# Optimization experiments

Measured on AMD Instinct MI355X. Metric: run time of the kernel, lower is better.

## Reference

```python
import jax, jax.numpy as jnp
import numpy as np

VOCAB = 32000
H = 256
B = 4
S = 512


def setup_inputs() -> dict:
    key = jax.random.key(0)
    ks = jax.random.split(key, 12)
    s = 1.0 / np.sqrt(H)
    inp = {
        "x": jax.random.randint(ks[0], (B, S), 0, VOCAB),
        "embed": jax.random.normal(ks[1], (VOCAB, H), jnp.float32) * 0.02,
        "Wi": jax.random.normal(ks[2], (H, H), jnp.float32) * s,   # i2h weight (in,out)
        "bi": jax.random.normal(ks[3], (H,), jnp.float32) * s,
        "Wh": jax.random.normal(ks[4], (H, H), jnp.float32) * s,   # h2h weight
        "bh": jax.random.normal(ks[5], (H,), jnp.float32) * s,
        "Wa": jax.random.normal(ks[6], (2 * H, H), jnp.float32) * s,  # attn_W (in=2H,out=H)
        "ba": jax.random.normal(ks[7], (H,), jnp.float32) * s,
        "va": jax.random.normal(ks[8], (H,), jnp.float32) * s,     # attn_v (no bias)
        "Wo": jax.random.normal(ks[9], (H, VOCAB), jnp.float32) * s,  # fc_out
        "bo": jax.random.normal(ks[10], (VOCAB,), jnp.float32) * s,
    }
    return inp


def _forward(x, embed, Wi, bi, Wh, bh, Wa, ba, va, Wo, bo):
    emb = embed[x]                               # [B,S,H]
    h0 = jnp.zeros((x.shape[0], H), emb.dtype)

    def step(h, e_t):
        h_new = jnp.tanh(e_t @ Wi + bi + h @ Wh + bh)
        return h_new, h_new

    _, hs = jax.lax.scan(step, h0, jnp.swapaxes(emb, 0, 1))  # [S,B,H]
    enc = jnp.swapaxes(hs, 0, 1)                 # [B,S,H] encoder states

    # Additive attention: energy(t,s) = tanh(W[ h_t ; h_s ] + b), score = v . energy
    Wq, Wk = Wa[:H], Wa[H:]
    q = enc @ Wq                                 # [B,S,H] (query = h_t half)
    k = enc @ Wk                                 # [B,S,H] (history half)
    energy = jnp.tanh(q[:, :, None, :] + k[:, None, :, :] + ba)  # [B,T,S,H]
    scores = jnp.einsum("btsh,h->bts", energy, va)

    seq = x.shape[1]
    causal = jnp.arange(seq)[None, :] < jnp.arange(seq)[:, None]  # [T,S]: s < t strictly
    weights = jax.nn.softmax(jnp.where(causal[None], scores, -1e9), axis=-1)
    ctx = jnp.einsum("bts,bsh->bth", weights, enc)               # [B,S,H]
    # t == 0: context = h_0 itself (no history)
    ctx = jnp.where((jnp.arange(seq) == 0)[None, :, None], enc[:, 0:1, :], ctx)

    out = (ctx + enc) @ Wo + bo                  # [B,S,V]
    return out, enc[:, -1, :]


def reference(x, embed, Wi, bi, Wh, bh, Wa, ba, va, Wo, bo):
    return _forward(x, embed, Wi, bi, Wh, bh, Wa, ba, va, Wo, bo)
```

## Files before the change

kernel.cpp:

```cpp
#include <hip/hip_runtime.h>
#include <hip/hip_bf16.h>
#include <hip/hip_fp16.h>

#define VOCAB 32000
#define H 256
#define B 4
#define S 512

typedef _Float16 f16x8 __attribute__((ext_vector_type(8)));
typedef short s16x8 __attribute__((ext_vector_type(8)));
typedef float f32x4 __attribute__((ext_vector_type(4)));

__device__ __forceinline__ float tanh_fast(float x) {
    float e = exp2f(x * 2.885390081777927f);
    return 1.0f - 2.0f * __builtin_amdgcn_rcpf(e + 1.0f);
}

__device__ __forceinline__ size_t fragIdx(int row, int h) {
    return ((size_t)((((row >> 4) * 8 + (h >> 5)) * 64) + ((h >> 3) & 3) * 16 + (row & 15)) << 3)
           + (h & 7);
}

__global__ __launch_bounds__(256) void k_wot(const float* __restrict__ Wo,
                                             ushort* __restrict__ WoTF) {
    __shared__ float tile[256][65];
    int n0 = blockIdx.x * 64;
    int tx = threadIdx.x & 63, ty = threadIdx.x >> 6;
#pragma unroll
    for (int i = 0; i < 64; ++i) {
        int k = i * 4 + ty;
        tile[k][tx] = Wo[(size_t)k * VOCAB + n0 + tx];
    }
    __syncthreads();
#pragma unroll
    for (int r = 0; r < 8; ++r) {
        int lin = threadIdx.x + 256 * r;
        int ll = lin & 15, lg = (lin >> 4) & 3, kk = (lin >> 6) & 7, nt = lin >> 9;
        int n = nt * 16 + ll;
        s16x8 v;
#pragma unroll
        for (int e = 0; e < 8; ++e) {
            __hip_bfloat16 b = __float2bfloat16(tile[kk * 32 + lg * 8 + e][n]);
            v[e] = *(short*)&b;
        }
        size_t unit = (size_t)(((n0 >> 4) + nt) * 8 + kk) * 64 + lg * 16 + ll;
        *(s16x8*)&WoTF[unit * 8] = v;
    }
}

__global__ void k_eprep(const int* __restrict__ x, const float* __restrict__ embed,
                        const float* __restrict__ Wi, const float* __restrict__ bi,
                        const float* __restrict__ bh, float* __restrict__ Ew) {
    int t = blockIdx.x, j = threadIdx.x;
    __shared__ float es[B][H];
    __shared__ int xs[B];
    if (j < B) xs[j] = x[j * S + t];
    __syncthreads();
    for (int b = 0; b < B; ++b) es[b][j] = embed[(size_t)xs[b] * H + j];
    float bias = bi[j] + bh[j];
    float a0 = bias, a1 = bias, a2 = bias, a3 = bias;
    __syncthreads();
    for (int i = 0; i < H; ++i) {
        float w = Wi[i * H + j];
        a0 += es[0][i] * w; a1 += es[1][i] * w;
        a2 += es[2][i] * w; a3 += es[3][i] * w;
    }
    f32x4 v; v[0] = a0; v[1] = a1; v[2] = a2; v[3] = a3;
    *(f32x4*)&Ew[(t * H + j) * 4] = v;
}

__global__ __launch_bounds__(256, 1) void k_rnn(const float* __restrict__ Ew,
                                                const float* __restrict__ Wh,
                                                _Float16* __restrict__ enc16,
                                                float* __restrict__ out_tail) {
    const int tid = threadIdx.x;
    const int w = tid >> 6;
    const int l = tid & 63;
    const int lg = l >> 4;
    const int ll = l & 15;

    __shared__ _Float16 hbuf[2][4][258];
    for (int idx = tid; idx < 2 * 4 * 258; idx += 256) (&hbuf[0][0][0])[idx] = (_Float16)0.f;

    f16x8 Bf[4][8];
#pragma unroll
    for (int nt = 0; nt < 4; ++nt) {
        int col = w * 64 + nt * 16 + ll;
#pragma unroll
        for (int kk = 0; kk < 8; ++kk) {
            int kb = kk * 32 + lg * 8;
            f16x8 v;
#pragma unroll
            for (int e = 0; e < 8; ++e) v[e] = (_Float16)Wh[(kb + e) * H + col];
            Bf[nt][kk] = v;
        }
    }
    __syncthreads();

    f32x4 eacc[2][4];
#pragma unroll
    for (int d = 0; d < 2; ++d)
#pragma unroll
        for (int nt = 0; nt < 4; ++nt) {
            int j = w * 64 + nt * 16 + ll;
            eacc[d][nt] = *(const f32x4*)&Ew[(d * H + j) * 4];
        }

    const int jcol = w * 64 + lg * 16 + ll;

    for (int t0 = 0; t0 < S; t0 += 2) {
#pragma unroll
        for (int u = 0; u < 2; ++u) {
            const int t = t0 + u;
            const int cur = u, nxt = u ^ 1;

            f16x8 Af[8];
#pragma unroll
            for (int kk = 0; kk < 8; ++kk)
                Af[kk] = *(const f16x8*)&hbuf[cur][l & 3][kk * 32 + lg * 8];

            f32x4 acc[4];
#pragma unroll
            for (int nt = 0; nt < 4; ++nt) acc[nt] = eacc[u][nt];

            {
                int tp = (t + 2 < S) ? t + 2 : S - 1;
#pragma unroll
                for (int nt = 0; nt < 4; ++nt) {
                    int j = w * 64 + nt * 16 + ll;
                    eacc[u][nt] = *(const f32x4*)&Ew[(tp * H + j) * 4];
                }
            }

#pragma unroll
            for (int kk = 0; kk < 8; ++kk)
#pragma unroll
                for (int nt = 0; nt < 4; ++nt)
                    acc[nt] = __builtin_amdgcn_mfma_f32_16x16x32_f16(Af[kk], Bf[nt][kk], acc[nt], 0, 0, 0);

            float v[4];
#pragma unroll
            for (int nt = 0; nt < 4; ++nt)
#pragma unroll
                for (int r = 0; r < 4; ++r) {
                    float tv = __shfl(acc[nt][r], ll);
                    if (lg == nt) v[r] = tv;
                }

            float hv[4];
#pragma unroll
            for (int r = 0; r < 4; ++r) hv[r] = tanh_fast(v[r]);

#pragma unroll
            for (int r = 0; r < 4; ++r) {
                _Float16 h16 = (_Float16)hv[r];
                hbuf[nxt][r][jcol] = h16;
                enc16[(r * S + t) * H + jcol] = h16;
            }
            if (t == S - 1) {
#pragma unroll
                for (int r = 0; r < 4; ++r) out_tail[r * H + jcol] = hv[r];
            }

            asm volatile("s_waitcnt lgkmcnt(0)" ::: "memory");
            __builtin_amdgcn_s_barrier();
            asm volatile("" ::: "memory");
        }
    }
}

__global__ void k_qk(const _Float16* __restrict__ enc16, const float* __restrict__ Wa,
                     const float* __restrict__ ba, float* __restrict__ q,
                     float* __restrict__ kT) {
    int r0 = blockIdx.x * 8;
    int j = threadIdx.x;
    __shared__ float es[8][H];
#pragma unroll
    for (int r = 0; r < 8; ++r) es[r][j] = (float)enc16[(r0 + r) * H + j];
    __syncthreads();
    float aq[8] = {0, 0, 0, 0, 0, 0, 0, 0};
    float ak[8] = {0, 0, 0, 0, 0, 0, 0, 0};
    for (int i = 0; i < H; ++i) {
        float wq = Wa[i * H + j];
        float wk = Wa[(H + i) * H + j];
#pragma unroll
        for (int r = 0; r < 8; ++r) { aq[r] += es[r][i] * wq; ak[r] += es[r][i] * wk; }
    }
    float bav = ba[j];
#pragma unroll
    for (int r = 0; r < 8; ++r) {
        int row = r0 + r;
        int b = row >> 9, t = row & (S - 1);
        q[row * H + j] = aq[r];
        kT[((b * H + j) << 9) + t] = ak[r] + bav;
    }
}

__global__ void k_attn(const float* __restrict__ q, const float* __restrict__ kT,
                       const _Float16* __restrict__ enc16, const float* __restrict__ va,
                       ushort* __restrict__ AbfF) {
    int bt = blockIdx.x;
    int b = bt >> 9, t = bt & (S - 1);
    int tid = threadIdx.x;
    if (t == 0) {
        float e = (float)enc16[(b * S) * H + tid];
        __hip_bfloat16 bf = __float2bfloat16(2.0f * e);
        AbfF[fragIdx(bt, tid)] = *(ushort*)&bf;
        return;
    }
    __shared__ float qs[H], vas[H], part[4][S], wgt[S], red[8];
    qs[tid] = q[bt * H + tid];
    vas[tid] = va[tid];
    __syncthreads();

    int sl = tid & 63, g = tid >> 6;
    int nchunk = (t + 63) >> 6;
    const float* kTb = kT + ((size_t)(b * H) << 9);
    for (int c = 0; c < nchunk; ++c) {
        int s = c * 64 + sl;
        float p = 0.f;
        if (s < t) {
            int hb = g * 64;
            for (int i = 0; i < 64; ++i) {
                int h = hb + i;
                p += vas[h] * tanh_fast(qs[h] + kTb[(h << 9) + s]);
            }
        }
        part[g][s] = p;
    }
    __syncthreads();

    float m = -1e30f;
    for (int s = tid; s < t; s += 256) {
        float sc = part[0][s] + part[1][s] + part[2][s] + part[3][s];
        wgt[s] = sc;
        m = fmaxf(m, sc);
    }
#pragma unroll
    for (int off = 32; off; off >>= 1) m = fmaxf(m, __shfl_xor(m, off));
    if ((tid & 63) == 0) red[g] = m;
    __syncthreads();
    m = fmaxf(fmaxf(red[0], red[1]), fmaxf(red[2], red[3]));
    float ssum = 0.f;
    for (int s = tid; s < t; s += 256) {
        float e = exp2f((wgt[s] - m) * 1.4426950408889634f);
        wgt[s] = e;
        ssum += e;
    }
#pragma unroll
    for (int off = 32; off; off >>= 1) ssum += __shfl_xor(ssum, off);
    if ((tid & 63) == 0) red[4 + g] = ssum;
    __syncthreads();
    float inv = 1.0f / (red[4] + red[5] + red[6] + red[7]);

    float ctx = 0.f;
    const _Float16* eb = enc16 + (size_t)(b * S) * H + tid;
    for (int s = 0; s < t; ++s) ctx += wgt[s] * (float)eb[s * H];
    float et = (float)enc16[(b * S + t) * H + tid];
    __hip_bfloat16 bf = __float2bfloat16(ctx * inv + et);
    AbfF[fragIdx(bt, tid)] = *(ushort*)&bf;
}

__global__ __launch_bounds__(256) void k_out(const ushort* __restrict__ AbfF,
                                             const ushort* __restrict__ WoTF,
                                             const float* __restrict__ bo,
                                             float* __restrict__ out) {
    int tid = threadIdx.x;
    int wv = tid >> 6, l = tid & 63;
    int mw = wv >> 1, nw = wv & 1;
    int lg = l >> 4, ll = l & 15;
    int m0 = blockIdx.y * 128 + mw * 64;
    int n0 = blockIdx.x * 128 + nw * 64;

    f32x4 acc[4][4];
#pragma unroll
    for (int mt = 0; mt < 4; ++mt)
#pragma unroll
        for (int nt = 0; nt < 4; ++nt) { f32x4 z; z[0]=0.f; z[1]=0.f; z[2]=0.f; z[3]=0.f; acc[mt][nt] = z; }

#pragma unroll
    for (int kk = 0; kk < 8; ++kk) {
        s16x8 a[4], bf[4];
#pragma unroll
        for (int mt = 0; mt < 4; ++mt)
            a[mt] = *(const s16x8*)&AbfF[((size_t)(((m0 >> 4) + mt) * 8 + kk) * 64 + l) * 8];
#pragma unroll
        for (int nt = 0; nt < 4; ++nt)
            bf[nt] = *(const s16x8*)&WoTF[((size_t)(((n0 >> 4) + nt) * 8 + kk) * 64 + l) * 8];
#pragma unroll
        for (int mt = 0; mt < 4; ++mt)
#pragma unroll
            for (int nt = 0; nt < 4; ++nt)
                acc[mt][nt] = __builtin_amdgcn_mfma_f32_16x16x32_bf16(a[mt], bf[nt], acc[mt][nt], 0, 0, 0);
    }

#pragma unroll
    for (int nt = 0; nt < 4; ++nt) {
        int n = n0 + nt * 16 + ll;
        float bov = bo[n];
#pragma unroll
        for (int mt = 0; mt < 4; ++mt) {
#pragma unroll
            for (int r = 0; r < 4; ++r) {
                int mrow = m0 + mt * 16 + lg * 4 + r;
                out[(size_t)mrow * VOCAB + n] = acc[mt][nt][r] + bov;
            }
        }
    }
}

extern "C" void kernel_launch(void* const* d_in, const int* in_sizes, int n_in,
                              void* d_out, int out_size, void* d_ws, size_t ws_size,
                              hipStream_t stream) {
    const int*   x     = (const int*)d_in[0];
    const float* embed = (const float*)d_in[1];
    const float* Wi    = (const float*)d_in[2];
    const float* bi    = (const float*)d_in[3];
    const float* Wh    = (const float*)d_in[4];
    const float* bh    = (const float*)d_in[5];
    const float* Wa    = (const float*)d_in[6];
    const float* ba    = (const float*)d_in[7];
    const float* va    = (const float*)d_in[8];
    const float* Wo    = (const float*)d_in[9];
    const float* bo    = (const float*)d_in[10];
    float* out = (float*)d_out;

    char* wsb = (char*)d_ws;
    float*    Ew    = (float*)(wsb);
    _Float16* enc16 = (_Float16*)(wsb + (2 << 20));
    float*    q     = (float*)(wsb + (3 << 20));
    float*    kT    = (float*)(wsb + (5 << 20));
    ushort*   AbfF  = (ushort*)(wsb + (7 << 20));
    ushort*   WoTF  = (ushort*)(wsb + (8 << 20));
    float* out_tail = out + (size_t)B * S * VOCAB;

    hipLaunchKernelGGL(k_wot,   dim3(VOCAB / 64),     dim3(256), 0, stream, Wo, WoTF);
    hipLaunchKernelGGL(k_eprep, dim3(S),              dim3(256), 0, stream, x, embed, Wi, bi, bh, Ew);
    hipLaunchKernelGGL(k_rnn,   dim3(1),              dim3(256), 0, stream, Ew, Wh, enc16, out_tail);
    hipLaunchKernelGGL(k_qk,    dim3(B * S / 8),      dim3(256), 0, stream, enc16, Wa, ba, q, kT);
    hipLaunchKernelGGL(k_attn,  dim3(B * S),          dim3(256), 0, stream, q, kT, enc16, va, AbfF);
    hipLaunchKernelGGL(k_out,   dim3(VOCAB / 128, (B * S) / 128), dim3(256), 0, stream, AbfF, WoTF, bo, out);
}
```

Baseline: 683.2 us.

## Move attention context into an MFMA kernel and reorder output GEMM grid

The attention kernel now writes normalized fp16 softmax weights in MFMA fragment layout, and a new k_ctx kernel computes the context as a weights×encoder matrix multiply using MFMA, adding the residual encoder state. This replaces the per-thread serial loop over history positions in k_attn. k_qk also emits the encoder in a fragment layout for this GEMM. The output GEMM grid is swapped so the M dimension varies fastest, for better reuse of the Wo tiles. The RNN step's shuffle-based extraction is replaced by a direct register select. That select looks like a possible correctness change, since it drops the cross-lane shuffle. Weights are rounded to fp16, which loses some precision.

```diff
diff --git a/kernel.cpp b/kernel.cpp
--- a/kernel.cpp
+++ b/kernel.cpp
@@ -140,12 +140,12 @@
 
             float v[4];
 #pragma unroll
-            for (int nt = 0; nt < 4; ++nt)
-#pragma unroll
-                for (int r = 0; r < 4; ++r) {
-                    float tv = __shfl(acc[nt][r], ll);
-                    if (lg == nt) v[r] = tv;
+            for (int nt = 0; nt < 4; ++nt) {
+                if (lg == nt) {
+#pragma unroll
+                    for (int r = 0; r < 4; ++r) v[r] = acc[nt][r];
                 }
+            }
 
             float hv[4];
 #pragma unroll
@@ -171,7 +171,7 @@
 
 __global__ void k_qk(const _Float16* __restrict__ enc16, const float* __restrict__ Wa,
                      const float* __restrict__ ba, float* __restrict__ q,
-                     float* __restrict__ kT) {
+                     float* __restrict__ kT, ushort* __restrict__ encF) {
     int r0 = blockIdx.x * 8;
     int j = threadIdx.x;
     __shared__ float es[8][H];
@@ -193,19 +193,23 @@
         int b = row >> 9, t = row & (S - 1);
         q[row * H + j] = aq[r];
         kT[((b * H + j) << 9) + t] = ak[r] + bav;
+        _Float16 ev = (_Float16)es[r][j];
+        size_t unit = (size_t)((b * 16 + (j >> 4)) * 16 + (t >> 5)) * 64 + ((t >> 3) & 3) * 16 + (j & 15);
+        encF[unit * 8 + (t & 7)] = *(ushort*)&ev;
     }
 }
 
 __global__ void k_attn(const float* __restrict__ q, const float* __restrict__ kT,
-                       const _Float16* __restrict__ enc16, const float* __restrict__ va,
-                       ushort* __restrict__ AbfF) {
+                       const float* __restrict__ va, ushort* __restrict__ WgtF) {
     int bt = blockIdx.x;
     int b = bt >> 9, t = bt & (S - 1);
     int tid = threadIdx.x;
     if (t == 0) {
-        float e = (float)enc16[(b * S) * H + tid];
-        __hip_bfloat16 bf = __float2bfloat16(2.0f * e);
-        AbfF[fragIdx(bt, tid)] = *(ushort*)&bf;
+        for (int ss = tid; ss < S; ss += 256) {
+            _Float16 hw = (_Float16)((ss == 0) ? 1.f : 0.f);
+            size_t unit = (size_t)((b * 32 + (t >> 4)) * 16 + (ss >> 5)) * 64 + ((ss >> 3) & 3) * 16 + (t & 15);
+            WgtF[unit * 8 + (ss & 7)] = *(ushort*)&hw;
+        }
         return;
     }
     __shared__ float qs[H], vas[H], part[4][S], wgt[S], red[8];
@@ -253,12 +257,58 @@
     __syncthreads();
     float inv = 1.0f / (red[4] + red[5] + red[6] + red[7]);
 
-    float ctx = 0.f;
-    const _Float16* eb = enc16 + (size_t)(b * S) * H + tid;
-    for (int s = 0; s < t; ++s) ctx += wgt[s] * (float)eb[s * H];
-    float et = (float)enc16[(b * S + t) * H + tid];
-    __hip_bfloat16 bf = __float2bfloat16(ctx * inv + et);
-    AbfF[fragIdx(bt, tid)] = *(ushort*)&bf;
+    for (int ss = tid; ss < S; ss += 256) {
+        float wv = (ss < t) ? wgt[ss] * inv : 0.f;
+        _Float16 hw = (_Float16)wv;
+        size_t unit = (size_t)((b * 32 + (t >> 4)) * 16 + (ss >> 5)) * 64 + ((ss >> 3) & 3) * 16 + (t & 15);
+        WgtF[unit * 8 + (ss & 7)] = *(ushort*)&hw;
+    }
+}
+
+__global__ __launch_bounds__(256) void k_ctx(const ushort* __restrict__ WgtF,
+                                             const ushort* __restrict__ encF,
+                                             const _Float16* __restrict__ enc16,
+                                             ushort* __restrict__ AbfF) {
+    int b = blockIdx.y;
+    int m0 = blockIdx.x * 32;
+    int tid = threadIdx.x;
+    int wv = tid >> 6, l = tid & 63;
+    int lg = l >> 4, ll = l & 15;
+
+    f32x4 acc[2][4];
+#pragma unroll
+    for (int mt = 0; mt < 2; ++mt)
+#pragma unroll
+        for (int nt = 0; nt < 4; ++nt) { f32x4 z; z[0]=0.f; z[1]=0.f; z[2]=0.f; z[3]=0.f; acc[mt][nt] = z; }
+
+#pragma unroll
+    for (int kk = 0; kk < 16; ++kk) {
+        f16x8 a[2], bf[4];
+#pragma unroll
+        for (int mt = 0; mt < 2; ++mt)
+            a[mt] = *(const f16x8*)&WgtF[((size_t)((b * 32 + (m0 >> 4) + mt) * 16 + kk) * 64 + l) * 8];
+#pragma unroll
+        for (int nt = 0; nt < 4; ++nt)
+            bf[nt] = *(const f16x8*)&encF[((size_t)((b * 16 + wv * 4 + nt) * 16 + kk) * 64 + l) * 8];
+#pragma unroll
+        for (int mt = 0; mt < 2; ++mt)
+#pragma unroll
+            for (int nt = 0; nt < 4; ++nt)
+                acc[mt][nt] = __builtin_amdgcn_mfma_f32_16x16x32_f16(a[mt], bf[nt], acc[mt][nt], 0, 0, 0);
+    }
+
+#pragma unroll
+    for (int mt = 0; mt < 2; ++mt)
+#pragma unroll
+        for (int nt = 0; nt < 4; ++nt)
+#pragma unroll
+            for (int r = 0; r < 4; ++r) {
+                int trow = m0 + mt * 16 + lg * 4 + r;
+                int h = wv * 64 + nt * 16 + ll;
+                float ev = (float)enc16[(size_t)(b * S + trow) * H + h];
+                __hip_bfloat16 o = __float2bfloat16(acc[mt][nt][r] + ev);
+                AbfF[fragIdx(b * S + trow, h)] = *(ushort*)&o;
+            }
 }
 
 __global__ __launch_bounds__(256) void k_out(const ushort* __restrict__ AbfF,
@@ -269,8 +319,8 @@
     int wv = tid >> 6, l = tid & 63;
     int mw = wv >> 1, nw = wv & 1;
     int lg = l >> 4, ll = l & 15;
-    int m0 = blockIdx.y * 128 + mw * 64;
-    int n0 = blockIdx.x * 128 + nw * 64;
+    int m0 = blockIdx.x * 128 + mw * 64;
+    int n0 = blockIdx.y * 128 + nw * 64;
 
     f32x4 acc[4][4];
 #pragma unroll
@@ -332,12 +382,15 @@
     float*    kT    = (float*)(wsb + (5 << 20));
     ushort*   AbfF  = (ushort*)(wsb + (7 << 20));
     ushort*   WoTF  = (ushort*)(wsb + (8 << 20));
+    ushort*   WgtF  = (ushort*)(wsb + (24 << 20));
+    ushort*   encF  = (ushort*)(wsb + (26 << 20));
     float* out_tail = out + (size_t)B * S * VOCAB;
 
     hipLaunchKernelGGL(k_wot,   dim3(VOCAB / 64),     dim3(256), 0, stream, Wo, WoTF);
     hipLaunchKernelGGL(k_eprep, dim3(S),              dim3(256), 0, stream, x, embed, Wi, bi, bh, Ew);
     hipLaunchKernelGGL(k_rnn,   dim3(1),              dim3(256), 0, stream, Ew, Wh, enc16, out_tail);
-    hipLaunchKernelGGL(k_qk,    dim3(B * S / 8),      dim3(256), 0, stream, enc16, Wa, ba, q, kT);
-    hipLaunchKernelGGL(k_attn,  dim3(B * S),          dim3(256), 0, stream, q, kT, enc16, va, AbfF);
-    hipLaunchKernelGGL(k_out,   dim3(VOCAB / 128, (B * S) / 128), dim3(256), 0, stream, AbfF, WoTF, bo, out);
-}
+    hipLaunchKernelGGL(k_qk,    dim3(B * S / 8),      dim3(256), 0, stream, enc16, Wa, ba, q, kT, encF);
+    hipLaunchKernelGGL(k_attn,  dim3(B * S),          dim3(256), 0, stream, q, kT, va, WgtF);
+    hipLaunchKernelGGL(k_ctx,   dim3(S / 32, B),      dim3(256), 0, stream, WgtF, encF, enc16, AbfF);
+    hipLaunchKernelGGL(k_out,   dim3(16, VOCAB / 128), dim3(256), 0, stream, AbfF, WoTF, bo, out);
+}
```

New measurement: 601.9 us. 11.9% less time.
